# Optimization experiments

Hardware: AMD Instinct MI355X
Metric: run time of the kernel (lower is better)

## Reference

```python
import jax, jax.numpy as jnp
import numpy as np

N, L, D = 1024, 128, 512
H = D // 2  # LSTM hidden per direction


def _lstm_dir(x, w_ih, w_hh, b_ih, b_hh, reverse=False):
    # x: [B, T, Din] -> [B, T, H]; PyTorch gate order i, f, g, o
    B = x.shape[0]
    Hh = w_hh.shape[1]
    xs = jnp.swapaxes(x, 0, 1)  # [T, B, Din]
    if reverse:
        xs = xs[::-1]
    pre = jnp.einsum('tbi,gi->tbg', xs, w_ih) + b_ih  # precompute input contribution

    def step(carry, p):
        h, c = carry
        g = p + h @ w_hh.T + b_hh
        i, f, cc, o = jnp.split(g, 4, axis=-1)
        c = jax.nn.sigmoid(f) * c + jax.nn.sigmoid(i) * jnp.tanh(cc)
        h = jax.nn.sigmoid(o) * jnp.tanh(c)
        return (h, c), h

    zeros = jnp.zeros((B, Hh), x.dtype)
    _, hs = jax.lax.scan(step, (zeros, zeros), pre)
    if reverse:
        hs = hs[::-1]
    return jnp.swapaxes(hs, 0, 1)


def _bilstm(x, params):
    # params: [(w_ih, w_hh, b_ih, b_hh)] for l0_fwd, l0_bwd, l1_fwd, l1_bwd
    for lf, lb in ((params[0], params[1]), (params[2], params[3])):
        f = _lstm_dir(x, *lf)
        b = _lstm_dir(x, *lb, reverse=True)
        x = jnp.concatenate([f, b], axis=-1)
    return x


def _forward(episodes, query, current_state, ages, Wq, bq, Wk, bk, lstm_params, k):
    # retrieve_relevant_episodes: batched version of the per-episode loop
    query_proj = query @ Wq.T + bq              # [D]
    emb = episodes.mean(axis=1)                 # [N, D] per-episode mean embedding
    key_proj = emb @ Wk.T + bk                  # [N, D]
    scores = key_proj @ query_proj              # [N] (matmul(q, kp.T).mean() == dot for 1D)
    _, idx = jax.lax.top_k(scores, k)           # descending, == argsort[-k:][::-1]
    sel = jnp.take(episodes, idx, axis=0)       # [k, L, D]
    # temporal_attention
    w = 1.0 / (1.0 + jnp.take(ages, idx) * 0.01)  # temporal recency weight
    x = sel * w[:, None, None]
    lstm_out = _bilstm(x, lstm_params)          # [k, L, D]
    att = jnp.einsum('d,kld->kl', current_state, lstm_out)  # [k, L] (== [k,1,L])
    attw = jax.nn.softmax(att, axis=-1)
    context = jnp.einsum('kl,kld->kd', attw, lstm_out)[:, None, :]  # [k, 1, D]
    return context


def setup_inputs() -> dict:
    key = jax.random.key(0)
    ks = jax.random.split(key, 32)
    s = 1.0 / np.sqrt(D)
    sh = 1.0 / np.sqrt(H)
    inp = {
        'episodes': jax.random.normal(ks[0], (N, L, D), jnp.float32),
        'query': jax.random.normal(ks[1], (D,), jnp.float32),
        'current_state': jax.random.normal(ks[2], (D,), jnp.float32),
        'ages': jax.random.uniform(ks[3], (N,), jnp.float32) * 100.0,
        'Wq': jax.random.normal(ks[4], (D, D), jnp.float32) * s,
        'bq': jnp.zeros((D,), jnp.float32),
        'Wk': jax.random.normal(ks[5], (D, D), jnp.float32) * s,
        'bk': jnp.zeros((D,), jnp.float32),
    }
    i = 6
    for name in ['l0', 'l0r', 'l1', 'l1r']:
        inp['w_ih_' + name] = jax.random.normal(ks[i], (4 * H, D), jnp.float32) * sh; i += 1
        inp['w_hh_' + name] = jax.random.normal(ks[i], (4 * H, H), jnp.float32) * sh; i += 1
        inp['b_ih_' + name] = jnp.zeros((4 * H,), jnp.float32)
        inp['b_hh_' + name] = jnp.zeros((4 * H,), jnp.float32)
    inp['k'] = 5
    return inp


def reference(episodes, query, current_state, ages, Wq, bq, Wk, bk,
              w_ih_l0, w_hh_l0, b_ih_l0, b_hh_l0,
              w_ih_l0r, w_hh_l0r, b_ih_l0r, b_hh_l0r,
              w_ih_l1, w_hh_l1, b_ih_l1, b_hh_l1,
              w_ih_l1r, w_hh_l1r, b_ih_l1r, b_hh_l1r, k):
    lstm_params = [
        (w_ih_l0, w_hh_l0, b_ih_l0, b_hh_l0),
        (w_ih_l0r, w_hh_l0r, b_ih_l0r, b_hh_l0r),
        (w_ih_l1, w_hh_l1, b_ih_l1, b_hh_l1),
        (w_ih_l1r, w_hh_l1r, b_ih_l1r, b_hh_l1r),
    ]
    return _forward(episodes, query, current_state, ages, Wq, bq, Wk, bk, lstm_params, k)
```

## Files before the change

### kernel.cpp

```cpp
#include <hip/hip_runtime.h>
#include <hip/hip_bf16.h>
#include <math.h>

typedef unsigned short u16;
typedef unsigned int   u32;
typedef unsigned long long u64;

#define DEV static __device__ __forceinline__

static constexpr int LL = 128, DD = 512, HH = 256, KK = 5, NN = 1024;

static constexpr size_t OFF_QP   = 0;
static constexpr size_t OFF_U    = 4096;
static constexpr size_t OFF_CC   = 8192;
static constexpr size_t OFF_SC   = 12288;
static constexpr size_t OFF_WSC  = 16384;
static constexpr size_t OFF_IDX  = 16640;
static constexpr size_t OFF_HG   = 20480;
static constexpr size_t OFF_PRE  = 102400;
static constexpr size_t OFF_OUT0 = OFF_PRE  + (size_t)2*LL*5*1024*4;
static constexpr size_t OFF_OUT1 = OFF_OUT0 + (size_t)5*LL*DD*4;

DEV float sigf(float x){ return 1.0f/(1.0f + expf(-x)); }

__global__ void k_qproj(const float* __restrict__ Wq, const float* __restrict__ q,
                        const float* __restrict__ bq, float* __restrict__ qp) {
  __shared__ float qs[512];
  int tid = threadIdx.x;
  qs[tid] = q[tid];
  __syncthreads();
  const float* row = Wq + (size_t)tid * 512;
  float acc = 0.f;
  for (int j = 0; j < 512; j += 4) {
    float4 w = *(const float4*)(row + j);
    acc += w.x * qs[j] + w.y * qs[j+1] + w.z * qs[j+2] + w.w * qs[j+3];
  }
  qp[tid] = acc + bq[tid];
}

__global__ void k_keyvec(const float* __restrict__ Wk, const float* __restrict__ bk,
                         const float* __restrict__ qp, float* __restrict__ u,
                         float* __restrict__ cconst) {
  __shared__ float qs[512];
  __shared__ float red[512];
  int tid = threadIdx.x;
  qs[tid] = qp[tid];
  __syncthreads();
  float acc = 0.f;
  for (int j = 0; j < 512; ++j) acc += Wk[(size_t)j*512 + tid] * qs[j];
  u[tid] = acc;
  red[tid] = bk[tid] * qs[tid];
  __syncthreads();
  for (int off = 256; off > 0; off >>= 1) { if (tid < off) red[tid] += red[tid+off]; __syncthreads(); }
  if (tid == 0) cconst[0] = red[0];
}

__global__ void k_scores(const float* __restrict__ ep, const float* __restrict__ u,
                         const float* __restrict__ cconst, float* __restrict__ scores) {
  __shared__ float red[256];
  int tid = threadIdx.x, n = blockIdx.x;
  int d0 = (tid * 4) & 511;
  float u0 = u[d0+0], u1 = u[d0+1], u2 = u[d0+2], u3 = u[d0+3];
  const float* base = ep + (size_t)n * (LL*DD);
  float acc = 0.f;
  for (int c = tid; c < (LL*DD)/4; c += 256) {
    float4 v = *(const float4*)(base + (size_t)c*4);
    acc += v.x*u0 + v.y*u1 + v.z*u2 + v.w*u3;
  }
  red[tid] = acc;
  __syncthreads();
  for (int off = 128; off > 0; off >>= 1) { if (tid < off) red[tid] += red[tid+off]; __syncthreads(); }
  if (tid == 0) scores[n] = red[0] * (1.0f/LL) + cconst[0];
}

__global__ void k_topk(const float* __restrict__ scores, const float* __restrict__ ages,
                       int* __restrict__ idx5, float* __restrict__ wsc) {
  __shared__ float s0[NN];
  __shared__ float sv[NN];
  __shared__ int   si[NN];
  __shared__ int   chosen[KK];
  int tid = threadIdx.x;
  s0[tid] = scores[tid];
  __syncthreads();
  for (int r = 0; r < KK; ++r) {
    float v = s0[tid];
    for (int m = 0; m < r; ++m) if (chosen[m] == tid) v = -3.4e38f;
    sv[tid] = v; si[tid] = tid;
    __syncthreads();
    for (int off = 512; off > 0; off >>= 1) {
      if (tid < off) {
        float a = sv[tid], b = sv[tid+off];
        int ia = si[tid], ib = si[tid+off];
        if (b > a || (b == a && ib < ia)) { sv[tid] = b; si[tid] = ib; }
      }
      __syncthreads();
    }
    if (tid == 0) {
      int w = si[0];
      chosen[r] = w;
      idx5[r] = w;
      wsc[r] = 1.0f / (1.0f + ages[w] * 0.01f);
    }
    __syncthreads();
  }
}

__global__ void k_pre(const float* __restrict__ ep, const float* __restrict__ x1,
                      const int* __restrict__ idx5, const float* __restrict__ wsc,
                      const float* __restrict__ wihF, const float* __restrict__ wihB,
                      const float* __restrict__ bihF, const float* __restrict__ bhhF,
                      const float* __restrict__ bihB, const float* __restrict__ bhhB,
                      float* __restrict__ pre) {
  int t = blockIdx.x, rb = blockIdx.y, dir = blockIdx.z;
  int tid = threadIdx.x;
  __shared__ __align__(16) float xs[5*512];
  __shared__ __align__(16) float wt[256*36];
  if (ep) {
    for (int f = tid; f < 5*512; f += 256) {
      int b = f >> 9, i = f & 511;
      xs[f] = ep[((size_t)idx5[b]*LL + t)*DD + i] * wsc[b];
    }
  } else {
    for (int f = tid; f < 5*512; f += 256) {
      int b = f >> 9, i = f & 511;
      xs[f] = x1[((size_t)b*LL + t)*DD + i];
    }
  }
  const float* wih = dir ? wihB : wihF;
  const float* bih = dir ? bihB : bihF;
  const float* bhh = dir ? bhhB : bhhF;
  int r0 = rb * 256;
  float acc[5] = {0,0,0,0,0};
  for (int it = 0; it < 16; ++it) {
    __syncthreads();
    for (int c = tid; c < 2048; c += 256) {
      int rr = c >> 3;
      int ii = (c & 7) * 4;
      *(float4*)&wt[rr*36 + ii] = *(const float4*)&wih[(size_t)(r0+rr)*512 + it*32 + ii];
    }
    __syncthreads();
    const float* wrow = &wt[(size_t)tid*36];
    const float* xb = &xs[it*32];
    for (int ii = 0; ii < 32; ii += 4) {
      float4 w = *(const float4*)(wrow + ii);
      #pragma unroll
      for (int b = 0; b < 5; ++b) {
        float4 xv = *(const float4*)&xb[b*512 + ii];
        acc[b] += w.x*xv.x + w.y*xv.y + w.z*xv.z + w.w*xv.w;
      }
    }
  }
  int grow = r0 + tid;
  float bias = bih[grow] + bhh[grow];
  size_t pbase = (((size_t)dir*LL + t)*5)*1024 + grow;
  #pragma unroll
  for (int b = 0; b < 5; ++b) pre[pbase + (size_t)b*1024] = acc[b] + bias;
}

__global__ __launch_bounds__(1024) void k_lstm(
    const float* __restrict__ whhF, const float* __restrict__ whhB,
    const float* __restrict__ pre, float* __restrict__ out,
    u64* __restrict__ hg) {
  int wg  = blockIdx.x;
  int dir = wg >> 3;
  int q   = wg & 7;
  int tid = threadIdx.x;
  int p   = tid & 127;
  int jq  = tid >> 7;
  int jb  = jq * 32;
  const float* whh = dir ? whhB : whhF;

  __shared__ __align__(16) float h_lds[5*256];
  __shared__ float part[128*5*9];
  __shared__ float c_s[5*32];
  __shared__ float pre_lds[2*5*128];

  int gr = (p >> 5) * 256 + q * 32 + (p & 31);
  float w[32];
  #pragma unroll
  for (int m4 = 0; m4 < 8; ++m4) {
    float4 a = *(const float4*)(whh + (size_t)gr*256 + jb + m4*4);
    w[m4*4+0] = a.x; w[m4*4+1] = a.y; w[m4*4+2] = a.z; w[m4*4+3] = a.w;
  }
  for (int f = tid; f < 1280; f += 1024) h_lds[f] = 0.f;
  if (tid < 160) c_s[tid] = 0.f;
  u64* hg_dir = hg + (size_t)dir * 2 * 1280;

  if (tid < 640) {
    int t0 = dir ? (LL-1) : 0;
    int b = tid >> 7, r = tid & 127;
    int grow = (r >> 5)*256 + q*32 + (r & 31);
    pre_lds[tid] = pre[(((size_t)dir*LL + t0)*5 + b)*1024 + grow];
  }
  __syncthreads();

  for (int s = 0; s < LL; ++s) {
    int par = s & 1;
    int t = dir ? (LL-1-s) : s;
    float acc[5];
    #pragma unroll
    for (int b = 0; b < 5; ++b) {
      const float4* h4 = (const float4*)&h_lds[b*256 + jb];
      float a = 0.f;
      #pragma unroll
      for (int m4 = 0; m4 < 8; ++m4) {
        float4 hv = h4[m4];
        a += w[m4*4+0]*hv.x + w[m4*4+1]*hv.y + w[m4*4+2]*hv.z + w[m4*4+3]*hv.w;
      }
      acc[b] = a;
    }
    #pragma unroll
    for (int b = 0; b < 5; ++b) part[(p*5 + b)*9 + jq] = acc[b];
    __syncthreads();
    if (tid < 160) {
      int b = tid >> 5, u = tid & 31;
      float g[4];
      #pragma unroll
      for (int gate = 0; gate < 4; ++gate) {
        int r = gate*32 + u;
        float sum = pre_lds[par*640 + b*128 + r];
        #pragma unroll
        for (int m = 0; m < 8; ++m) sum += part[(r*5 + b)*9 + m];
        g[gate] = sum;
      }
      float ig = sigf(g[0]), fg = sigf(g[1]), cc = tanhf(g[2]), og = sigf(g[3]);
      float cn = fg * c_s[b*32 + u] + ig * cc;
      c_s[b*32 + u] = cn;
      float hv = og * tanhf(cn);
      out[((size_t)b*LL + t)*DD + dir*HH + q*32 + u] = hv;
      u64* hwr = hg_dir + (size_t)((s + 1) & 1) * 1280;
      u64 pk = ((u64)(u32)(s + 1) << 32) | (u64)__float_as_uint(hv);
      __hip_atomic_store(&hwr[b*256 + q*32 + u], pk,
                         __ATOMIC_RELAXED, __HIP_MEMORY_SCOPE_AGENT);
    } else if (tid >= 256 && tid < 896 && s + 1 < LL) {
      int f = tid - 256;
      int b = f >> 7, r = f & 127;
      int tn = dir ? (LL-2-s) : (s+1);
      int grow = (r >> 5)*256 + q*32 + (r & 31);
      pre_lds[(par^1)*640 + f] = pre[(((size_t)dir*LL + tn)*5 + b)*1024 + grow];
    }
    if (s + 1 < LL) {
      int sp = s + 1;
      const u64* hrd = hg_dir + (size_t)(sp & 1) * 1280;
      for (int f = tid; f < 1280; f += 1024) {
        u64 v = __hip_atomic_load(&hrd[f], __ATOMIC_RELAXED,
                                  __HIP_MEMORY_SCOPE_AGENT);
        while ((u32)(v >> 32) != (u32)sp) {
          v = __hip_atomic_load(&hrd[f], __ATOMIC_RELAXED,
                                __HIP_MEMORY_SCOPE_AGENT);
        }
        h_lds[f] = __uint_as_float((u32)v);
      }
    }
    __syncthreads();
  }
}

__global__ void k_attn(const float* __restrict__ out1, const float* __restrict__ csb,
                       float* __restrict__ outp) {
  int b = blockIdx.x, tid = threadIdx.x;
  __shared__ float cs[512];
  __shared__ float att[128];
  __shared__ float red[256];
  __shared__ float smax, ssum;
  cs[tid] = csb[tid]; cs[tid+256] = csb[tid+256];
  __syncthreads();
  {
    int t = tid & 127, half = tid >> 7;
    const float* row = out1 + ((size_t)b*LL + t)*DD + half*256;
    const float* c2 = cs + half*256;
    float a = 0.f;
    for (int d = 0; d < 256; ++d) a += row[d] * c2[d];
    red[tid] = a;
  }
  __syncthreads();
  if (tid < 128) att[tid] = red[tid] + red[tid+128];
  __syncthreads();
  if (tid < 64) red[tid] = fmaxf(att[tid], att[tid+64]);
  __syncthreads();
  if (tid == 0) { float m = red[0]; for (int o = 1; o < 64; ++o) m = fmaxf(m, red[o]); smax = m; }
  __syncthreads();
  if (tid < 128) att[tid] = expf(att[tid] - smax);
  __syncthreads();
  if (tid < 64) red[tid] = att[tid] + att[tid+64];
  __syncthreads();
  if (tid == 0) { float s = 0.f; for (int o = 0; o < 64; ++o) s += red[o]; ssum = s; }
  __syncthreads();
  float inv = 1.0f / ssum;
  for (int d = tid; d < DD; d += 256) {
    float acc = 0.f;
    for (int t2 = 0; t2 < LL; ++t2) acc += att[t2] * out1[((size_t)b*LL + t2)*DD + d];
    outp[b*DD + d] = acc * inv;
  }
}

extern "C" void kernel_launch(void* const* d_in, const int* in_sizes, int n_in,
                              void* d_out, int out_size, void* d_ws, size_t ws_size,
                              hipStream_t stream) {
  (void)in_sizes; (void)n_in; (void)out_size; (void)ws_size;
  const float* ep   = (const float*)d_in[0];
  const float* qu   = (const float*)d_in[1];
  const float* cst  = (const float*)d_in[2];
  const float* ages = (const float*)d_in[3];
  const float* Wq   = (const float*)d_in[4];
  const float* bq   = (const float*)d_in[5];
  const float* Wk   = (const float*)d_in[6];
  const float* bk   = (const float*)d_in[7];
  const float *wih[4], *whh[4], *bih[4], *bhh[4];
  for (int l = 0; l < 4; ++l) {
    wih[l] = (const float*)d_in[8 + l*4 + 0];
    whh[l] = (const float*)d_in[8 + l*4 + 1];
    bih[l] = (const float*)d_in[8 + l*4 + 2];
    bhh[l] = (const float*)d_in[8 + l*4 + 3];
  }
  char* ws = (char*)d_ws;
  float* qp   = (float*)(ws + OFF_QP);
  float* uvec = (float*)(ws + OFF_U);
  float* cc   = (float*)(ws + OFF_CC);
  float* sc   = (float*)(ws + OFF_SC);
  float* wsc  = (float*)(ws + OFF_WSC);
  int*   idx5 = (int*)  (ws + OFF_IDX);
  u64*   hg0  = (u64*)  (ws + OFF_HG);
  u64*   hg1  = (u64*)  (ws + OFF_HG + 40960);
  float* pre  = (float*)(ws + OFF_PRE);
  float* out0 = (float*)(ws + OFF_OUT0);
  float* out1 = (float*)(ws + OFF_OUT1);

  hipMemsetAsync(ws + OFF_HG, 0, 81920, stream);

  k_qproj <<<1, 512, 0, stream>>>(Wq, qu, bq, qp);
  k_keyvec<<<1, 512, 0, stream>>>(Wk, bk, qp, uvec, cc);
  k_scores<<<NN, 256, 0, stream>>>(ep, uvec, cc, sc);
  k_topk  <<<1, 1024, 0, stream>>>(sc, ages, idx5, wsc);

  k_pre <<<dim3(LL,4,2), 256, 0, stream>>>(ep, nullptr, idx5, wsc,
        wih[0], wih[1], bih[0], bhh[0], bih[1], bhh[1], pre);
  k_lstm<<<16, 1024, 0, stream>>>(whh[0], whh[1], pre, out0, hg0);

  k_pre <<<dim3(LL,4,2), 256, 0, stream>>>(nullptr, out0, idx5, wsc,
        wih[2], wih[3], bih[2], bhh[2], bih[3], bhh[3], pre);
  k_lstm<<<16, 1024, 0, stream>>>(whh[2], whh[3], pre, out1, hg1);

  k_attn<<<KK, 256, 0, stream>>>(out1, cst, (float*)d_out);
}
```

Baseline: 1.548 ms.

## Spread query/key projections across blocks and tighten LSTM step polling

The query projection and key-vector kernels previously ran as single blocks; they are now split across 64 and 32 blocks, using warp-shuffle and shared-memory partial reductions. This removes a serialized single-CU read of two 512x512 weight matrices. In the recurrent LSTM kernel, each step now writes its own hidden values straight to LDS. It also issues the next-step pre-activation load into a register before spinning on the hidden-state flags, and polls two slots per thread concurrently. These changes aim to shorten per-step latency on the critical recurrence, at the cost of more complex spin logic and some benign duplicate LDS writes.

```diff
diff --git a/kernel.cpp b/kernel.cpp
--- a/kernel.cpp
+++ b/kernel.cpp
@@ -27,32 +27,51 @@
                         const float* __restrict__ bq, float* __restrict__ qp) {
   __shared__ float qs[512];
   int tid = threadIdx.x;
-  qs[tid] = q[tid];
-  __syncthreads();
-  const float* row = Wq + (size_t)tid * 512;
+  qs[tid] = q[tid]; qs[tid+256] = q[tid+256];
+  __syncthreads();
+  int row  = blockIdx.x*8 + (tid >> 5);
+  int lane = tid & 31;
+  const float* wr = Wq + (size_t)row*512 + lane*16;
   float acc = 0.f;
-  for (int j = 0; j < 512; j += 4) {
-    float4 w = *(const float4*)(row + j);
-    acc += w.x * qs[j] + w.y * qs[j+1] + w.z * qs[j+2] + w.w * qs[j+3];
-  }
-  qp[tid] = acc + bq[tid];
+  #pragma unroll
+  for (int j = 0; j < 16; j += 4) {
+    float4 w = *(const float4*)(wr + j);
+    acc += w.x*qs[lane*16+j] + w.y*qs[lane*16+j+1] + w.z*qs[lane*16+j+2] + w.w*qs[lane*16+j+3];
+  }
+  #pragma unroll
+  for (int off = 16; off > 0; off >>= 1) acc += __shfl_down(acc, off, 32);
+  if (lane == 0) qp[row] = acc + bq[row];
 }
 
 __global__ void k_keyvec(const float* __restrict__ Wk, const float* __restrict__ bk,
                          const float* __restrict__ qp, float* __restrict__ u,
                          float* __restrict__ cconst) {
   __shared__ float qs[512];
-  __shared__ float red[512];
-  int tid = threadIdx.x;
-  qs[tid] = qp[tid];
-  __syncthreads();
+  __shared__ float red[16][17];
+  __shared__ float r2[256];
+  int tid = threadIdx.x;
+  qs[tid] = qp[tid]; qs[tid+256] = qp[tid+256];
+  __syncthreads();
+  int cl = tid & 15;
+  int jc = tid >> 4;
+  int col = blockIdx.x*16 + cl;
   float acc = 0.f;
-  for (int j = 0; j < 512; ++j) acc += Wk[(size_t)j*512 + tid] * qs[j];
-  u[tid] = acc;
-  red[tid] = bk[tid] * qs[tid];
-  __syncthreads();
-  for (int off = 256; off > 0; off >>= 1) { if (tid < off) red[tid] += red[tid+off]; __syncthreads(); }
-  if (tid == 0) cconst[0] = red[0];
+  for (int j = jc*32; j < jc*32 + 32; ++j) acc += Wk[(size_t)j*512 + col] * qs[j];
+  red[cl][jc] = acc;
+  __syncthreads();
+  if (tid < 16) {
+    float a = 0.f;
+    #pragma unroll
+    for (int m = 0; m < 16; ++m) a += red[tid][m];
+    u[blockIdx.x*16 + tid] = a;
+  }
+  if (blockIdx.x == 0) {
+    float b2 = bk[tid]*qs[tid] + bk[tid+256]*qs[tid+256];
+    r2[tid] = b2;
+    __syncthreads();
+    for (int off = 128; off > 0; off >>= 1) { if (tid < off) r2[tid] += r2[tid+off]; __syncthreads(); }
+    if (tid == 0) cconst[0] = r2[0];
+  }
 }
 
 __global__ void k_scores(const float* __restrict__ ep, const float* __restrict__ u,
@@ -225,33 +244,46 @@
       }
       float ig = sigf(g[0]), fg = sigf(g[1]), cc = tanhf(g[2]), og = sigf(g[3]);
       float cn = fg * c_s[b*32 + u] + ig * cc;
-      c_s[b*32 + u] = cn;
       float hv = og * tanhf(cn);
-      out[((size_t)b*LL + t)*DD + dir*HH + q*32 + u] = hv;
       u64* hwr = hg_dir + (size_t)((s + 1) & 1) * 1280;
       u64 pk = ((u64)(u32)(s + 1) << 32) | (u64)__float_as_uint(hv);
       __hip_atomic_store(&hwr[b*256 + q*32 + u], pk,
                          __ATOMIC_RELAXED, __HIP_MEMORY_SCOPE_AGENT);
-    } else if (tid >= 256 && tid < 896 && s + 1 < LL) {
+      c_s[b*32 + u] = cn;
+      out[((size_t)b*LL + t)*DD + dir*HH + q*32 + u] = hv;
+      h_lds[b*256 + q*32 + u] = hv;
+    }
+    float pfv = 0.f; int pfok = 0;
+    if (tid >= 256 && tid < 896 && s + 1 < LL) {
       int f = tid - 256;
       int b = f >> 7, r = f & 127;
       int tn = dir ? (LL-2-s) : (s+1);
       int grow = (r >> 5)*256 + q*32 + (r & 31);
-      pre_lds[(par^1)*640 + f] = pre[(((size_t)dir*LL + tn)*5 + b)*1024 + grow];
-    }
-    if (s + 1 < LL) {
+      pfv = pre[(((size_t)dir*LL + tn)*5 + b)*1024 + grow];
+      pfok = 1;
+    }
+    if (tid >= 160 && s + 1 < LL) {
       int sp = s + 1;
       const u64* hrd = hg_dir + (size_t)(sp & 1) * 1280;
-      for (int f = tid; f < 1280; f += 1024) {
-        u64 v = __hip_atomic_load(&hrd[f], __ATOMIC_RELAXED,
-                                  __HIP_MEMORY_SCOPE_AGENT);
-        while ((u32)(v >> 32) != (u32)sp) {
-          v = __hip_atomic_load(&hrd[f], __ATOMIC_RELAXED,
-                                __HIP_MEMORY_SCOPE_AGENT);
+      int f0 = tid - 160;
+      int f1 = f0 + 864;
+      bool has2 = (f1 < 1280);
+      u64 v0 = __hip_atomic_load(&hrd[f0], __ATOMIC_RELAXED, __HIP_MEMORY_SCOPE_AGENT);
+      u64 v1 = has2 ? __hip_atomic_load(&hrd[f1], __ATOMIC_RELAXED, __HIP_MEMORY_SCOPE_AGENT)
+                    : 0ull;
+      bool d0 = false, d1 = !has2;
+      while (!(d0 && d1)) {
+        if (!d0) {
+          if ((u32)(v0 >> 32) == (u32)sp) { h_lds[f0] = __uint_as_float((u32)v0); d0 = true; }
+          else v0 = __hip_atomic_load(&hrd[f0], __ATOMIC_RELAXED, __HIP_MEMORY_SCOPE_AGENT);
         }
-        h_lds[f] = __uint_as_float((u32)v);
-      }
-    }
+        if (!d1) {
+          if ((u32)(v1 >> 32) == (u32)sp) { h_lds[f1] = __uint_as_float((u32)v1); d1 = true; }
+          else v1 = __hip_atomic_load(&hrd[f1], __ATOMIC_RELAXED, __HIP_MEMORY_SCOPE_AGENT);
+        }
+      }
+    }
+    if (pfok) pre_lds[((par^1))*640 + (tid - 256)] = pfv;
     __syncthreads();
   }
 }
@@ -328,8 +360,8 @@
 
   hipMemsetAsync(ws + OFF_HG, 0, 81920, stream);
 
-  k_qproj <<<1, 512, 0, stream>>>(Wq, qu, bq, qp);
-  k_keyvec<<<1, 512, 0, stream>>>(Wk, bk, qp, uvec, cc);
+  k_qproj <<<64, 256, 0, stream>>>(Wq, qu, bq, qp);
+  k_keyvec<<<32, 256, 0, stream>>>(Wk, bk, qp, uvec, cc);
   k_scores<<<NN, 256, 0, stream>>>(ep, uvec, cc, sc);
   k_topk  <<<1, 1024, 0, stream>>>(sc, ages, idx5, wsc);
 
```

Measured after the change: 1.525 ms. No clear change (-1.5%).
